# Optimization experiments

Measured on AMD Instinct MI355X. Metric: run time of the kernel, lower is better.

Reference implementation:

```python
import jax, jax.numpy as jnp
import numpy as np
import math

B, S, H = 2, 1024, 768
NH = 12
DH = H // NH  # 64


def _heads(t):
    # (B,S,H) -> (B,NH,S,DH)
    b, s, _ = t.shape
    return t.reshape(b, s, NH, DH).transpose(0, 2, 1, 3)


def _merge(t):
    # (B,NH,S,DH) -> (B,S,H)
    b, nh, s, dh = t.shape
    return t.transpose(0, 2, 1, 3).reshape(b, s, nh * dh)


def _forward(x, y, vq_w, vq_b, vk_w, vk_b, vv_w, vv_b,
             dq_w, dq_b, dk_w, dk_b, dv_w, dv_b,
             van_fc_w, van_fc_b, WD_w, d_theta_w, d_theta_b, WV_w,
             diff_fc_w, diff_fc_b, v_gamma_w, v_gamma_b,
             diff_out_w, diff_out_b, van_out_w, van_out_b,
             diff_fus_w, diff_fus_b, van_fus_w, van_fus_b,
             gate_w, nf_w, nf_b, nf_out_w, final_w, final_b):
    scale = 1.0 / math.sqrt(DH)

    # ---- Vanilla attention (dropout is eval-mode identity) ----
    q = _heads(x @ vq_w + vq_b)
    k = _heads(y @ vk_w + vk_b)
    v = _heads(y @ vv_w + vv_b)
    scores = jnp.einsum('bhid,bhjd->bhij', q, k) * scale
    probs = jax.nn.softmax(scores, axis=-1)
    van_vector = _merge(jnp.einsum('bhij,bhjd->bhid', probs, v))

    # ---- Differential attention ----
    # scores[b,h,i,j] = sum_d (q[b,h,i,d] - k[b,h,i,d]) / sqrt(DH)  (constant over j,
    # due to the module's broadcast indexing). Keep explicit softmax for exact math/vjp.
    dq = _heads(x @ dq_w + dq_b)
    dk = _heads(y @ dk_w + dk_b)
    dv = _heads(y @ dv_w + dv_b)
    s_row = (dq.sum(-1) - dk.sum(-1)) * scale  # (B,NH,S)
    d_scores = jnp.broadcast_to(s_row[..., None], s_row.shape + (s_row.shape[-1],))
    d_probs = jax.nn.softmax(d_scores, axis=-1)
    diff_vector = _merge(jnp.einsum('bhij,bhjd->bhid', d_probs, dv))

    # ---- Coupled gating (SoftMax over dim=1 == sequence axis) ----
    theta = jnp.tanh(jnp.concatenate((diff_vector @ WD_w, x_lin(van_vector, van_fc_w, van_fc_b)), axis=-1))
    d_theta = diff_vector * jax.nn.softmax(theta @ d_theta_w + d_theta_b, axis=1)
    gamma = jnp.tanh(jnp.concatenate((van_vector @ WV_w, d_theta @ diff_fc_w + diff_fc_b), axis=-1))
    a_gamma = van_vector * jax.nn.softmax(gamma @ v_gamma_w + v_gamma_b, axis=1)
    diff_out = jnp.tanh(jnp.concatenate((diff_vector, d_theta), axis=-1) @ diff_out_w + diff_out_b)
    van_out = jnp.tanh(jnp.concatenate((van_vector, a_gamma), axis=-1) @ van_out_w + van_out_b)
    diff_fusion = jnp.tanh(diff_out @ diff_fus_w + diff_fus_b)
    van_fusion = jnp.tanh(van_out @ van_fus_w + van_fus_b)
    gate = jax.nn.sigmoid(jnp.concatenate((diff_fusion, van_fusion), axis=-1) @ gate_w)  # (B,S,1)
    fusion = gate * van_fusion + (1.0 - gate) * diff_fusion
    nf = jax.nn.sigmoid(jnp.concatenate((van_vector, fusion @ nf_w + nf_b), axis=-1) @ nf_out_w)
    return nf * jnp.tanh(fusion @ final_w + final_b)


def x_lin(t, w, b):
    return t @ w + b


def setup_inputs() -> dict:
    key = jax.random.key(0)
    ks = iter(jax.random.split(key, 64))
    def w(*shape):
        return jax.random.normal(next(ks), shape, jnp.float32) * 0.02
    def b(n):
        return jnp.zeros((n,), jnp.float32)
    inp = {
        'x': jax.random.normal(next(ks), (B, S, H), jnp.float32),
        'y': jax.random.normal(next(ks), (B, S, H), jnp.float32),
        'vq_w': w(H, H), 'vq_b': b(H), 'vk_w': w(H, H), 'vk_b': b(H), 'vv_w': w(H, H), 'vv_b': b(H),
        'dq_w': w(H, H), 'dq_b': b(H), 'dk_w': w(H, H), 'dk_b': b(H), 'dv_w': w(H, H), 'dv_b': b(H),
        'van_fc_w': w(H, H), 'van_fc_b': b(H),
        'WD_w': w(H, H),
        'd_theta_w': w(2 * H, H), 'd_theta_b': b(H),
        'WV_w': w(H, H),
        'diff_fc_w': w(H, H), 'diff_fc_b': b(H),
        'v_gamma_w': w(2 * H, H), 'v_gamma_b': b(H),
        'diff_out_w': w(2 * H, H), 'diff_out_b': b(H),
        'van_out_w': w(2 * H, H), 'van_out_b': b(H),
        'diff_fus_w': w(H, H), 'diff_fus_b': b(H),
        'van_fus_w': w(H, H), 'van_fus_b': b(H),
        'gate_w': w(2 * H, 1),
        'nf_w': w(H, H), 'nf_b': b(H),
        'nf_out_w': w(2 * H, 1),
        'final_w': w(H, H), 'final_b': b(H),
    }
    return inp


def reference(x, y, vq_w, vq_b, vk_w, vk_b, vv_w, vv_b,
              dq_w, dq_b, dk_w, dk_b, dv_w, dv_b,
              van_fc_w, van_fc_b, WD_w, d_theta_w, d_theta_b, WV_w,
              diff_fc_w, diff_fc_b, v_gamma_w, v_gamma_b,
              diff_out_w, diff_out_b, van_out_w, van_out_b,
              diff_fus_w, diff_fus_b, van_fus_w, van_fus_b,
              gate_w, nf_w, nf_b, nf_out_w, final_w, final_b):
    return _forward(x, y, vq_w, vq_b, vk_w, vk_b, vv_w, vv_b,
                    dq_w, dq_b, dk_w, dk_b, dv_w, dv_b,
                    van_fc_w, van_fc_b, WD_w, d_theta_w, d_theta_b, WV_w,
                    diff_fc_w, diff_fc_b, v_gamma_w, v_gamma_b,
                    diff_out_w, diff_out_b, van_out_w, van_out_b,
                    diff_fus_w, diff_fus_b, van_fus_w, van_fus_b,
                    gate_w, nf_w, nf_b, nf_out_w, final_w, final_b)
```

## Files before the change

kernel.cpp:

```cpp
#include <hip/hip_runtime.h>
#include <hip/hip_bf16.h>
#include <math.h>

#define H 768
#define S 1024
#define BATCH 2
#define T 2048
#define TH ((size_t)T * H)

typedef unsigned short u16;
typedef __attribute__((ext_vector_type(8))) short short8;
typedef __attribute__((ext_vector_type(4))) float f32x4;

__device__ __forceinline__ u16 f2b(float f) {
  __hip_bfloat16 h = __float2bfloat16(f);
  return *reinterpret_cast<u16*>(&h);
}
__device__ __forceinline__ float b2f(u16 u) {
  __hip_bfloat16 h = *reinterpret_cast<__hip_bfloat16*>(&u);
  return __bfloat162float(h);
}
__device__ __forceinline__ void gload16(const u16* g, u16* lds) {
  __builtin_amdgcn_global_load_lds((const __attribute__((address_space(1))) void*)g,
                                   (__attribute__((address_space(3))) void*)lds, 16, 0, 0);
}

__global__ __launch_bounds__(256) void cvt2_k(const float* __restrict__ X, const float* __restrict__ Y,
                                              u16* __restrict__ OX, u16* __restrict__ OY) {
  const float* src = blockIdx.y ? Y : X;
  u16* dst = blockIdx.y ? OY : OX;
  int i = blockIdx.x * 256 + threadIdx.x;
  float4 a = ((const float4*)src)[2 * i];
  float4 b = ((const float4*)src)[2 * i + 1];
  u16 tmp[8] = {f2b(a.x), f2b(a.y), f2b(a.z), f2b(a.w), f2b(b.x), f2b(b.y), f2b(b.z), f2b(b.w)};
  ((uint4*)dst)[i] = *(uint4*)tmp;
}

struct WprepArgs {
  const float* src[14];
  unsigned dst[14];
  int ktiles[14];
  int tstart[15];
};
__global__ __launch_bounds__(256) void wprep_k(WprepArgs a, u16* __restrict__ wt) {
  __shared__ float sT[64][68];
  int blk = blockIdx.x;
  int mi = 0;
  while (blk >= a.tstart[mi + 1]) ++mi;
  int local = blk - a.tstart[mi];
  int kt = a.ktiles[mi];
  int tn = local / kt, tk = local % kt;
  int K = kt * 64;
  const float* W = a.src[mi];
  u16* D = wt + a.dst[mi];
  int t = threadIdx.x;
  int r = t >> 2, c = (t & 3) * 16;
  const float4* srcp = (const float4*)(W + ((size_t)(tk * 64 + r)) * H + tn * 64 + c);
  float4 v0 = srcp[0], v1 = srcp[1], v2 = srcp[2], v3 = srcp[3];
  *(float4*)&sT[r][c] = v0; *(float4*)&sT[r][c + 4] = v1;
  *(float4*)&sT[r][c + 8] = v2; *(float4*)&sT[r][c + 12] = v3;
  __syncthreads();
  int n = t >> 2, kk = (t & 3) * 16;
  u16 tmp[16];
  #pragma unroll
  for (int j = 0; j < 16; ++j) tmp[j] = f2b(sT[kk + j][n]);
  uint4* dst = (uint4*)(D + ((size_t)(tn * 64 + n)) * K + tk * 64 + kk);
  dst[0] = *(uint4*)&tmp[0];
  dst[1] = *(uint4*)&tmp[8];
}

__global__ __launch_bounds__(256) void meany1_k(const float* __restrict__ Y, float* __restrict__ part) {
  int blk = blockIdx.x;
  int b = blk / 24, r = blk % 24, cc = r / 8, sc = r % 8;
  int c = cc * 256 + threadIdx.x;
  const float* yp = Y + (size_t)b * S * H + (size_t)sc * 128 * H + c;
  float s = 0.f;
  for (int j = 0; j < 128; ++j) s += yp[(size_t)j * H];
  part[(sc * 2 + b) * H + c] = s;
}
__global__ __launch_bounds__(256) void meany2_k(const float* __restrict__ part, float* __restrict__ ybar) {
  int t = blockIdx.x * 256 + threadIdx.x;
  float s = 0.f;
  int b = t / H, c = t % H;
  #pragma unroll
  for (int sc = 0; sc < 8; ++sc) s += part[(sc * 2 + b) * H + c];
  ybar[t] = s * (1.0f / 1024.0f);
}

__global__ __launch_bounds__(256) void gemv_k(const float* __restrict__ A, const float* __restrict__ W,
                                              const float* __restrict__ bias, float* __restrict__ O, int act) {
  int gid = blockIdx.x * 4 + (threadIdx.x >> 6);
  int lane = threadIdx.x & 63;
  int b = gid / H, n = gid % H;
  const float* a = A + b * H;
  float s = 0.f;
  #pragma unroll
  for (int i = 0; i < 12; ++i) {
    int k = lane + 64 * i;
    s = fmaf(a[k], W[(size_t)k * H + n], s);
  }
  #pragma unroll
  for (int off = 32; off; off >>= 1) s += __shfl_xor(s, off);
  if (lane == 0) {
    if (bias) s += bias[n];
    if (act) s = tanhf(s);
    O[gid] = s;
  }
}

struct Reg {
  const u16 *A, *W, *A2, *W2;
  const float *bias, *perbatch;
  u16* Cb; u16* CbT; float* Cf;
  int ldw, ldw2;
};
struct GArgs { Reg r0, r1, r2; int act; };

__global__ __launch_bounds__(256) void bgemm_k(GArgs ga) {
  __shared__ u16 sA[3][64 * 64];
  __shared__ u16 sB[3][64 * 64];
  int t = threadIdx.x;
  int ri = blockIdx.x / 12;
  Reg R;
  if (ri == 0) R = ga.r0; else if (ri == 1) R = ga.r1; else R = ga.r2;
  int n0 = (blockIdx.x % 12) * 64;
  int m0 = blockIdx.y * 64;
  int w = t >> 6, l = t & 63, lr = l & 15, lg = l >> 4;
  int wr = (w >> 1) * 32, wc = (w & 1) * 32;

  f32x4 acc[2][2];
  #pragma unroll
  for (int i = 0; i < 2; ++i)
    #pragma unroll
    for (int j = 0; j < 2; ++j) acc[i][j] = (f32x4){0.f, 0.f, 0.f, 0.f};

  int NT = R.A2 ? 24 : 12;

  auto stage = [&](int ti) {
    int bi = ti % 3;
    const u16* Aq = (ti < 12) ? R.A : R.A2;
    const u16* Wq = (ti < 12) ? R.W : R.W2;
    int ldwq = (ti < 12) ? R.ldw : R.ldw2;
    int k0 = (ti % 12) * 64;
    #pragma unroll
    for (int ii = 0; ii < 2; ++ii) {
      int chunk = w * 128 + ii * 64 + l;
      int rr = chunk >> 3, c8 = chunk & 7;
      gload16(Aq + (size_t)(m0 + rr) * H + k0 + 8 * (c8 ^ (rr & 7)), &sA[bi][0] + (w * 128 + ii * 64) * 8);
      gload16(Wq + (size_t)(n0 + rr) * ldwq + k0 + 8 * (c8 ^ (rr & 7)), &sB[bi][0] + (w * 128 + ii * 64) * 8);
    }
  };

  stage(0);
  stage(1);
  for (int kt = 0; kt < NT; ++kt) {
    if (kt + 1 < NT) asm volatile("s_waitcnt vmcnt(4)" ::: "memory");
    else             asm volatile("s_waitcnt vmcnt(0)" ::: "memory");
    __builtin_amdgcn_s_barrier();
    if (kt + 2 < NT) stage(kt + 2);
    const u16* sAv = &sA[kt % 3][0];
    const u16* sBv = &sB[kt % 3][0];
    #pragma unroll
    for (int kh = 0; kh < 2; ++kh) {
      short8 af[2], bfr[2];
      #pragma unroll
      for (int mi = 0; mi < 2; ++mi) {
        int row = wr + 16 * mi + lr;
        af[mi] = *(const short8*)(sAv + row * 64 + 8 * ((4 * kh + lg) ^ (row & 7)));
      }
      #pragma unroll
      for (int ni = 0; ni < 2; ++ni) {
        int row = wc + 16 * ni + lr;
        bfr[ni] = *(const short8*)(sBv + row * 64 + 8 * ((4 * kh + lg) ^ (row & 7)));
      }
      #pragma unroll
      for (int mi = 0; mi < 2; ++mi)
        #pragma unroll
        for (int ni = 0; ni < 2; ++ni)
          acc[mi][ni] = __builtin_amdgcn_mfma_f32_16x16x32_bf16(af[mi], bfr[ni], acc[mi][ni], 0, 0, 0);
    }
  }

  #pragma unroll
  for (int mi = 0; mi < 2; ++mi) {
    #pragma unroll
    for (int ni = 0; ni < 2; ++ni) {
      int col = n0 + wc + 16 * ni + lr;
      u16 tmp4[4];
      #pragma unroll
      for (int reg = 0; reg < 4; ++reg) {
        int row = m0 + wr + 16 * mi + lg * 4 + reg;
        int bb = row >> 10;
        float v = acc[mi][ni][reg];
        if (R.bias) v += R.bias[col];
        if (R.perbatch) v += R.perbatch[bb * H + col];
        if (ga.act) v = tanhf(v);
        if (R.Cb) R.Cb[(size_t)row * H + col] = f2b(v);
        if (R.Cf) R.Cf[(size_t)row * H + col] = v;
        tmp4[reg] = f2b(v);
      }
      if (R.CbT) {
        int row0 = m0 + wr + 16 * mi + lg * 4;
        int bb = row0 >> 10, tok = row0 & 1023, hh = col >> 6, dd = col & 63;
        *(unsigned long long*)&R.CbT[((size_t)((bb * 12 + hh) * 64 + dd)) * 1024 + tok] =
            *(unsigned long long*)tmp4;
      }
    }
  }
}

__global__ __launch_bounds__(256) void mattn_k(
    const u16* __restrict__ Q, const u16* __restrict__ Kg,
    const u16* __restrict__ VT, u16* __restrict__ O)
{
  __shared__ u16 sK[3][64 * 64];
  __shared__ u16 sV[3][64 * 64];
  __shared__ u16 sQ[64 * 64];
  __shared__ u16 sP[4 * 16 * 64];
  int t = threadIdx.x;
  int w = t >> 6, l = t & 63, lr = l & 15, lg = l >> 4;
  int blk = blockIdx.x;
  int b = blk / 192; int rem = blk % 192; int h = rem / 16; int q0 = (rem % 16) * 64;

  #pragma unroll
  for (int i = 0; i < 2; ++i) {
    int id = t + i * 256; int r = id >> 3, c = id & 7;
    uint4 v = *(const uint4*)(Q + ((size_t)(b * 1024 + q0 + r)) * H + h * 64 + 8 * c);
    *(uint4*)(&sQ[0] + r * 64 + 8 * (c ^ (r & 7))) = v;
  }
  asm volatile("s_waitcnt lgkmcnt(0)" ::: "memory");

  auto stageKV = [&](int ti) {
    int bi = ti % 3;
    int kv0 = ti * 64;
    #pragma unroll
    for (int ii = 0; ii < 2; ++ii) {
      int chunk = w * 128 + ii * 64 + l;
      int rr = chunk >> 3, c8 = chunk & 7;
      gload16(Kg + ((size_t)(b * 1024 + kv0 + rr)) * H + h * 64 + 8 * (c8 ^ (rr & 7)),
              &sK[bi][0] + (w * 128 + ii * 64) * 8);
      gload16(VT + ((size_t)((b * 12 + h) * 64 + rr)) * 1024 + kv0 + 8 * (c8 ^ (rr & 7)),
              &sV[bi][0] + (w * 128 + ii * 64) * 8);
    }
  };

  f32x4 oacc[4];
  #pragma unroll
  for (int i = 0; i < 4; ++i) oacc[i] = (f32x4){0.f, 0.f, 0.f, 0.f};
  float lsum[4] = {0.f, 0.f, 0.f, 0.f};

  stageKV(0);
  stageKV(1);

  for (int kt = 0; kt < 16; ++kt) {
    if (kt + 1 < 16) asm volatile("s_waitcnt vmcnt(4)" ::: "memory");
    else             asm volatile("s_waitcnt vmcnt(0)" ::: "memory");
    __builtin_amdgcn_s_barrier();
    if (kt + 2 < 16) stageKV(kt + 2);
    const u16* sKv = &sK[kt % 3][0];
    const u16* sVv = &sV[kt % 3][0];

    f32x4 sacc[4];
    #pragma unroll
    for (int i = 0; i < 4; ++i) sacc[i] = (f32x4){0.f, 0.f, 0.f, 0.f};
    #pragma unroll
    for (int kh = 0; kh < 2; ++kh) {
      int qrow = 16 * w + lr;
      short8 qf = *(const short8*)(&sQ[0] + qrow * 64 + 8 * ((4 * kh + lg) ^ (qrow & 7)));
      #pragma unroll
      for (int ns = 0; ns < 4; ++ns) {
        int krow = 16 * ns + lr;
        short8 kf = *(const short8*)(sKv + krow * 64 + 8 * ((4 * kh + lg) ^ (krow & 7)));
        sacc[ns] = __builtin_amdgcn_mfma_f32_16x16x32_bf16(qf, kf, sacc[ns], 0, 0, 0);
      }
    }

    #pragma unroll
    for (int r = 0; r < 4; ++r) {
      int q = lg * 4 + r;
      #pragma unroll
      for (int ns = 0; ns < 4; ++ns) {
        float p = __expf(sacc[ns][r] * 0.125f);
        lsum[r] += p;
        int kv = 16 * ns + lr;
        unsigned byteoff = (unsigned)(w * 2048 + q * 128 + ((kv * 2) ^ ((q & 7) << 4)));
        *(u16*)((char*)sP + byteoff) = f2b(p);
      }
    }

    #pragma unroll
    for (int kh = 0; kh < 2; ++kh) {
      short8 pf = *(const short8*)((char*)sP + w * 2048 + lr * 128 + (((4 * kh + lg) << 4) ^ ((lr & 7) << 4)));
      #pragma unroll
      for (int ds = 0; ds < 4; ++ds) {
        int vrow = 16 * ds + lr;
        short8 vf = *(const short8*)(sVv + vrow * 64 + 8 * ((4 * kh + lg) ^ (vrow & 7)));
        oacc[ds] = __builtin_amdgcn_mfma_f32_16x16x32_bf16(pf, vf, oacc[ds], 0, 0, 0);
      }
    }
  }

  #pragma unroll
  for (int r = 0; r < 4; ++r) {
    #pragma unroll
    for (int off = 1; off < 16; off <<= 1) lsum[r] += __shfl_xor(lsum[r], off);
    float inv = 1.0f / lsum[r];
    int qrow = q0 + 16 * w + lg * 4 + r;
    #pragma unroll
    for (int ds = 0; ds < 4; ++ds) {
      int d = 16 * ds + lr;
      O[((size_t)(b * 1024 + qrow)) * H + h * 64 + d] = f2b(oacc[ds][r] * inv);
    }
  }
}

__global__ __launch_bounds__(256) void colsmP_k(const u16* __restrict__ Z, float* __restrict__ part) {
  int blk = blockIdx.x;
  int b = blk >> 7, sc = blk & 127;
  int t = threadIdx.x;
  const u16* zp = Z + ((size_t)(b * 1024 + sc * 8)) * H;
  float a0 = 0.f, a1 = 0.f, a2 = 0.f;
  #pragma unroll
  for (int j = 0; j < 8; ++j) {
    a0 += __expf(b2f(zp[(size_t)j * H + t]));
    a1 += __expf(b2f(zp[(size_t)j * H + t + 256]));
    a2 += __expf(b2f(zp[(size_t)j * H + t + 512]));
  }
  float* pp = part + (size_t)blk * H;
  pp[t] = a0; pp[t + 256] = a1; pp[t + 512] = a2;
}
__global__ __launch_bounds__(256) void colsmC_k(const float* __restrict__ part, float* __restrict__ inv) {
  int idx = blockIdx.x * 256 + threadIdx.x;
  int b = idx / H, c = idx % H;
  float s = 0.f;
  for (int sc = 0; sc < 128; ++sc) s += part[(size_t)(b * 128 + sc) * H + c];
  inv[idx] = 1.0f / s;
}
__global__ __launch_bounds__(256) void colsmA_k(
    const u16* __restrict__ Z, const float* __restrict__ inv,
    const float* __restrict__ mulvec, const u16* __restrict__ mulmat, u16* __restrict__ O) {
  int blk = blockIdx.x;
  int b = blk >> 7, sc = blk & 127;
  int t = threadIdx.x;
  size_t base = ((size_t)(b * 1024 + sc * 8)) * H;
  float i0 = inv[b * H + t], i1 = inv[b * H + t + 256], i2 = inv[b * H + t + 512];
  float m0 = 0.f, m1 = 0.f, m2 = 0.f;
  if (mulvec) { m0 = mulvec[b * H + t]; m1 = mulvec[b * H + t + 256]; m2 = mulvec[b * H + t + 512]; }
  #pragma unroll
  for (int j = 0; j < 8; ++j) {
    size_t row = base + (size_t)j * H;
    float e0 = __expf(b2f(Z[row + t]));
    float e1 = __expf(b2f(Z[row + t + 256]));
    float e2 = __expf(b2f(Z[row + t + 512]));
    float u0 = mulmat ? b2f(mulmat[row + t]) : m0;
    float u1 = mulmat ? b2f(mulmat[row + t + 256]) : m1;
    float u2 = mulmat ? b2f(mulmat[row + t + 512]) : m2;
    O[row + t] = f2b(u0 * e0 * i0);
    O[row + t + 256] = f2b(u1 * e1 * i1);
    O[row + t + 512] = f2b(u2 * e2 * i2);
  }
}

__global__ __launch_bounds__(256) void gatefuse_k(
    const u16* __restrict__ DF, const u16* __restrict__ VF,
    const float* __restrict__ GW, u16* __restrict__ FU)
{
  __shared__ float red[256];
  int tok = blockIdx.x;
  int t = threadIdx.x;
  const u16* df = DF + (size_t)tok * H;
  const u16* vf = VF + (size_t)tok * H;
  float dv[3], vv[3];
  float p = 0.f;
  #pragma unroll
  for (int i = 0; i < 3; ++i) {
    int c = t + i * 256;
    dv[i] = b2f(df[c]); vv[i] = b2f(vf[c]);
    p = fmaf(dv[i], GW[c], p);
    p = fmaf(vv[i], GW[H + c], p);
  }
  red[t] = p; __syncthreads();
  for (int st = 128; st; st >>= 1) { if (t < st) red[t] += red[t + st]; __syncthreads(); }
  float g = 1.0f / (1.0f + __expf(-red[0]));
  u16* fu = FU + (size_t)tok * H;
  #pragma unroll
  for (int i = 0; i < 3; ++i) {
    int c = t + i * 256;
    fu[c] = f2b(g * vv[i] + (1.0f - g) * dv[i]);
  }
}

__global__ __launch_bounds__(256) void nffinal_k(
    const u16* __restrict__ VAN, const float* __restrict__ NP,
    const float* __restrict__ NW, const float* __restrict__ FP,
    float* __restrict__ OUT)
{
  __shared__ float red[256];
  int tok = blockIdx.x;
  int t = threadIdx.x;
  const u16* va = VAN + (size_t)tok * H;
  const float* np = NP + (size_t)tok * H;
  float p = 0.f;
  #pragma unroll
  for (int i = 0; i < 3; ++i) {
    int c = t + i * 256;
    p = fmaf(b2f(va[c]), NW[c], p);
    p = fmaf(np[c], NW[H + c], p);
  }
  red[t] = p; __syncthreads();
  for (int st = 128; st; st >>= 1) { if (t < st) red[t] += red[t + st]; __syncthreads(); }
  float nf = 1.0f / (1.0f + __expf(-red[0]));
  const float* fp = FP + (size_t)tok * H;
  float* o = OUT + (size_t)tok * H;
  #pragma unroll
  for (int i = 0; i < 3; ++i) {
    int c = t + i * 256;
    o[c] = nf * tanhf(fp[c]);
  }
}

extern "C" void kernel_launch(void* const* d_in, const int* in_sizes, int n_in,
                              void* d_out, int out_size, void* d_ws, size_t ws_size,
                              hipStream_t stream) {
  const float* x        = (const float*)d_in[0];
  const float* y        = (const float*)d_in[1];
  const float* vq_w     = (const float*)d_in[2];
  const float* vq_b     = (const float*)d_in[3];
  const float* vk_w     = (const float*)d_in[4];
  const float* vk_b     = (const float*)d_in[5];
  const float* vv_w     = (const float*)d_in[6];
  const float* vv_b     = (const float*)d_in[7];
  const float* dv_w     = (const float*)d_in[12];
  const float* dv_b     = (const float*)d_in[13];
  const float* van_fc_w = (const float*)d_in[14];
  const float* van_fc_b = (const float*)d_in[15];
  const float* d_theta_w= (const float*)d_in[17];
  const float* WV_w     = (const float*)d_in[19];
  const float* diff_fc_w= (const float*)d_in[20];
  const float* diff_fc_b= (const float*)d_in[21];
  const float* v_gamma_w= (const float*)d_in[22];
  const float* diff_out_w=(const float*)d_in[24];
  const float* diff_out_b=(const float*)d_in[25];
  const float* van_out_w= (const float*)d_in[26];
  const float* van_out_b= (const float*)d_in[27];
  const float* diff_fus_w=(const float*)d_in[28];
  const float* diff_fus_b=(const float*)d_in[29];
  const float* van_fus_w= (const float*)d_in[30];
  const float* van_fus_b= (const float*)d_in[31];
  const float* gate_w   = (const float*)d_in[32];
  const float* nf_w     = (const float*)d_in[33];
  const float* nf_b     = (const float*)d_in[34];
  const float* nf_out_w = (const float*)d_in[35];
  const float* final_w  = (const float*)d_in[36];
  const float* final_b  = (const float*)d_in[37];
  float* out = (float*)d_out;

  u16* wt = (u16*)d_ws;
  const size_t HH_ = (size_t)H * H;
  const size_t HH2 = 2 * HH_;
  size_t woff[14];
  const float* wsrc[14] = {vq_w, vk_w, vv_w, van_fc_w, WV_w, diff_fc_w, diff_fus_w, van_fus_w,
                           nf_w, final_w, d_theta_w, v_gamma_w, diff_out_w, van_out_w};
  int wk[14] = {12,12,12,12,12,12,12,12,12,12, 24,24,24,24};
  size_t o = 0;
  for (int i = 0; i < 14; ++i) { woff[i] = o; o += (i < 10) ? HH_ : HH2; }
  u16* bufs = wt + o;
  u16* bX   = bufs + 0 * TH;
  u16* bY   = bufs + 1 * TH;
  u16* bQ   = bufs + 2 * TH;
  u16* bK   = bufs + 3 * TH;
  u16* bV   = bufs + 4 * TH;
  u16* bVT  = bufs + 5 * TH;
  u16* bVan = bufs + 6 * TH;
  float* F0 = (float*)(bufs + 7 * TH);
  float* F1 = F0 + TH;
  float* sm = F1 + TH;
  float* ybar  = sm;
  float* dvbar = sm + 1536;
  float* c2    = sm + 3072;
  float* part  = sm + 4608;
  float* colp  = sm + 4608 + 12288;
  float* cinv  = colp + 196608;

  WprepArgs wa;
  int ts = 0;
  for (int i = 0; i < 14; ++i) {
    wa.src[i] = wsrc[i];
    wa.dst[i] = (unsigned)woff[i];
    wa.ktiles[i] = wk[i];
    wa.tstart[i] = ts;
    ts += wk[i] * 12;
  }
  wa.tstart[14] = ts;
  wprep_k<<<ts, 256, 0, stream>>>(wa, wt);
  cvt2_k<<<dim3(TH / 8 / 256, 2), 256, 0, stream>>>(x, y, bX, bY);

  meany1_k<<<48, 256, 0, stream>>>(y, part);
  meany2_k<<<6, 256, 0, stream>>>(part, ybar);
  gemv_k<<<384, 256, 0, stream>>>(ybar, dv_w, dv_b, dvbar, 0);
  gemv_k<<<384, 256, 0, stream>>>(dvbar, diff_out_w, diff_out_b, c2, 0);

  const u16 *wt_vq = wt + woff[0], *wt_vk = wt + woff[1], *wt_vv = wt + woff[2],
            *wt_vanfc = wt + woff[3], *wt_WV = wt + woff[4], *wt_difffc = wt + woff[5],
            *wt_difffus = wt + woff[6], *wt_vanfus = wt + woff[7], *wt_nf = wt + woff[8],
            *wt_final = wt + woff[9], *wt_dtheta = wt + woff[10], *wt_vg = wt + woff[11],
            *wt_diffout = wt + woff[12], *wt_vanout = wt + woff[13];
  #define NO nullptr
  Reg RZ = {NO, NO, NO, NO, NO, NO, NO, NO, NO, 0, 0};

  {
    GArgs g;
    g.r0 = {bX, wt_vq, NO, NO, vq_b, NO, bQ, NO, NO, H, 0};
    g.r1 = {bY, wt_vk, NO, NO, vk_b, NO, bK, NO, NO, H, 0};
    g.r2 = {bY, wt_vv, NO, NO, vv_b, NO, NO, bVT, NO, H, 0};
    g.act = 0;
    bgemm_k<<<dim3(36, 32), 256, 0, stream>>>(g);
  }
  mattn_k<<<384, 256, 0, stream>>>(bQ, bK, bVT, bVan);

  {
    GArgs g;
    g.r0 = {bVan, wt_vanfc, NO, NO, van_fc_b, NO, bX, NO, NO, H, 0};
    g.r1 = {bVan, wt_WV, NO, NO, NO, NO, bK, NO, NO, H, 0};
    g.r2 = RZ;
    g.act = 1;
    bgemm_k<<<dim3(24, 32), 256, 0, stream>>>(g);
  }
  {
    GArgs g;
    g.r0 = {bX, wt_dtheta + H, NO, NO, NO, NO, bY, NO, NO, 2 * H, 0};
    g.r1 = RZ; g.r2 = RZ;
    g.act = 0;
    bgemm_k<<<dim3(12, 32), 256, 0, stream>>>(g);
  }
  colsmP_k<<<256, 256, 0, stream>>>(bY, colp);
  colsmC_k<<<6, 256, 0, stream>>>(colp, cinv);
  colsmA_k<<<256, 256, 0, stream>>>(bY, cinv, dvbar, NO, bQ);
  {
    GArgs g;
    g.r0 = {bQ, wt_difffc, NO, NO, diff_fc_b, NO, bV, NO, NO, H, 0};
    g.r1 = {bQ, wt_diffout + H, NO, NO, NO, c2, bY, NO, NO, 2 * H, 0};
    g.r2 = RZ;
    g.act = 1;
    bgemm_k<<<dim3(24, 32), 256, 0, stream>>>(g);
  }
  {
    GArgs g;
    g.r0 = {bK, wt_vg, bV, wt_vg + H, NO, NO, bX, NO, NO, 2 * H, 2 * H};
    g.r1 = RZ; g.r2 = RZ;
    g.act = 0;
    bgemm_k<<<dim3(12, 32), 256, 0, stream>>>(g);
  }
  colsmP_k<<<256, 256, 0, stream>>>(bX, colp);
  colsmC_k<<<6, 256, 0, stream>>>(colp, cinv);
  colsmA_k<<<256, 256, 0, stream>>>(bX, cinv, NO, bVan, bX);
  {
    GArgs g;
    g.r0 = {bVan, wt_vanout, bX, wt_vanout + H, van_out_b, NO, bK, NO, NO, 2 * H, 2 * H};
    g.r1 = {bY, wt_difffus, NO, NO, diff_fus_b, NO, bQ, NO, NO, H, 0};
    g.r2 = RZ;
    g.act = 1;
    bgemm_k<<<dim3(24, 32), 256, 0, stream>>>(g);
  }
  {
    GArgs g;
    g.r0 = {bK, wt_vanfus, NO, NO, van_fus_b, NO, bV, NO, NO, H, 0};
    g.r1 = RZ; g.r2 = RZ;
    g.act = 1;
    bgemm_k<<<dim3(12, 32), 256, 0, stream>>>(g);
  }
  gatefuse_k<<<T, 256, 0, stream>>>(bQ, bV, gate_w, bY);
  {
    GArgs g;
    g.r0 = {bY, wt_nf, NO, NO, nf_b, NO, NO, NO, F0, H, 0};
    g.r1 = {bY, wt_final, NO, NO, final_b, NO, NO, NO, F1, H, 0};
    g.r2 = RZ;
    g.act = 0;
    bgemm_k<<<dim3(24, 32), 256, 0, stream>>>(g);
  }
  nffinal_k<<<T, 256, 0, stream>>>(bVan, F0, nf_out_w, F1, out);
}
```

Baseline: 252.7 us.

## Fuse column-softmax partial sums into GEMM epilogue and drop two kernels

The GEMM epilogue now computes exp of each bf16-rounded output and reduces it per column across the tile, writing per-64-row partial sums. The apply kernel folds the remaining 32-way reduction and the reciprocal inline. This removes the separate partial-sum and combine kernels, along with an extra read of the logits matrix, in both softmax stages. In exchange the apply kernel repeats the 32-partial reduction in every block, and the GEMM epilogue does extra exp work.

New measurement: 232.9 us. -7.8%, faster.

```diff
diff --git a/kernel.cpp b/kernel.cpp
--- a/kernel.cpp
+++ b/kernel.cpp
@@ -111,7 +111,7 @@
 struct Reg {
   const u16 *A, *W, *A2, *W2;
   const float *bias, *perbatch;
-  u16* Cb; u16* CbT; float* Cf;
+  u16* Cb; u16* CbT; float* Cf; float* colPart;
   int ldw, ldw2;
 };
 struct GArgs { Reg r0, r1, r2; int act; };
@@ -181,6 +181,7 @@
     }
   }
 
+  float ps[2] = {0.f, 0.f};
   #pragma unroll
   for (int mi = 0; mi < 2; ++mi) {
     #pragma unroll
@@ -195,15 +196,28 @@
         if (R.bias) v += R.bias[col];
         if (R.perbatch) v += R.perbatch[bb * H + col];
         if (ga.act) v = tanhf(v);
-        if (R.Cb) R.Cb[(size_t)row * H + col] = f2b(v);
+        tmp4[reg] = f2b(v);
+        if (R.Cb) R.Cb[(size_t)row * H + col] = tmp4[reg];
         if (R.Cf) R.Cf[(size_t)row * H + col] = v;
-        tmp4[reg] = f2b(v);
+        if (R.colPart) ps[ni] += __expf(b2f(tmp4[reg]));
       }
       if (R.CbT) {
         int row0 = m0 + wr + 16 * mi + lg * 4;
         int bb = row0 >> 10, tok = row0 & 1023, hh = col >> 6, dd = col & 63;
         *(unsigned long long*)&R.CbT[((size_t)((bb * 12 + hh) * 64 + dd)) * 1024 + tok] =
             *(unsigned long long*)tmp4;
+      }
+    }
+  }
+  if (R.colPart) {
+    #pragma unroll
+    for (int ni = 0; ni < 2; ++ni) {
+      float p = ps[ni];
+      p += __shfl_xor(p, 16);
+      p += __shfl_xor(p, 32);
+      if (lg == 0) {
+        int col = n0 + wc + 16 * ni + lr;
+        R.colPart[(size_t)(blockIdx.y * 2 + (wr >> 5)) * H + col] = p;
       }
     }
   }
@@ -314,36 +328,19 @@
   }
 }
 
-__global__ __launch_bounds__(256) void colsmP_k(const u16* __restrict__ Z, float* __restrict__ part) {
-  int blk = blockIdx.x;
-  int b = blk >> 7, sc = blk & 127;
-  int t = threadIdx.x;
-  const u16* zp = Z + ((size_t)(b * 1024 + sc * 8)) * H;
-  float a0 = 0.f, a1 = 0.f, a2 = 0.f;
-  #pragma unroll
-  for (int j = 0; j < 8; ++j) {
-    a0 += __expf(b2f(zp[(size_t)j * H + t]));
-    a1 += __expf(b2f(zp[(size_t)j * H + t + 256]));
-    a2 += __expf(b2f(zp[(size_t)j * H + t + 512]));
-  }
-  float* pp = part + (size_t)blk * H;
-  pp[t] = a0; pp[t + 256] = a1; pp[t + 512] = a2;
-}
-__global__ __launch_bounds__(256) void colsmC_k(const float* __restrict__ part, float* __restrict__ inv) {
-  int idx = blockIdx.x * 256 + threadIdx.x;
-  int b = idx / H, c = idx % H;
-  float s = 0.f;
-  for (int sc = 0; sc < 128; ++sc) s += part[(size_t)(b * 128 + sc) * H + c];
-  inv[idx] = 1.0f / s;
-}
 __global__ __launch_bounds__(256) void colsmA_k(
-    const u16* __restrict__ Z, const float* __restrict__ inv,
+    const u16* __restrict__ Z, const float* __restrict__ part,
     const float* __restrict__ mulvec, const u16* __restrict__ mulmat, u16* __restrict__ O) {
   int blk = blockIdx.x;
   int b = blk >> 7, sc = blk & 127;
   int t = threadIdx.x;
+  float s0 = 0.f, s1 = 0.f, s2 = 0.f;
+  for (int i = b * 32; i < b * 32 + 32; ++i) {
+    const float* pp = part + (size_t)i * H;
+    s0 += pp[t]; s1 += pp[t + 256]; s2 += pp[t + 512];
+  }
+  float i0 = 1.0f / s0, i1 = 1.0f / s1, i2 = 1.0f / s2;
   size_t base = ((size_t)(b * 1024 + sc * 8)) * H;
-  float i0 = inv[b * H + t], i1 = inv[b * H + t + 256], i2 = inv[b * H + t + 512];
   float m0 = 0.f, m1 = 0.f, m2 = 0.f;
   if (mulvec) { m0 = mulvec[b * H + t]; m1 = mulvec[b * H + t + 256]; m2 = mulvec[b * H + t + 512]; }
   #pragma unroll
@@ -480,7 +477,6 @@
   float* c2    = sm + 3072;
   float* part  = sm + 4608;
   float* colp  = sm + 4608 + 12288;
-  float* cinv  = colp + 196608;
 
   WprepArgs wa;
   int ts = 0;
@@ -506,13 +502,13 @@
             *wt_final = wt + woff[9], *wt_dtheta = wt + woff[10], *wt_vg = wt + woff[11],
             *wt_diffout = wt + woff[12], *wt_vanout = wt + woff[13];
   #define NO nullptr
-  Reg RZ = {NO, NO, NO, NO, NO, NO, NO, NO, NO, 0, 0};
-
-  {
-    GArgs g;
-    g.r0 = {bX, wt_vq, NO, NO, vq_b, NO, bQ, NO, NO, H, 0};
-    g.r1 = {bY, wt_vk, NO, NO, vk_b, NO, bK, NO, NO, H, 0};
-    g.r2 = {bY, wt_vv, NO, NO, vv_b, NO, NO, bVT, NO, H, 0};
+  Reg RZ = {NO, NO, NO, NO, NO, NO, NO, NO, NO, NO, 0, 0};
+
+  {
+    GArgs g;
+    g.r0 = {bX, wt_vq, NO, NO, vq_b, NO, bQ, NO, NO, NO, H, 0};
+    g.r1 = {bY, wt_vk, NO, NO, vk_b, NO, bK, NO, NO, NO, H, 0};
+    g.r2 = {bY, wt_vv, NO, NO, vv_b, NO, NO, bVT, NO, NO, H, 0};
     g.act = 0;
     bgemm_k<<<dim3(36, 32), 256, 0, stream>>>(g);
   }
@@ -520,51 +516,47 @@
 
   {
     GArgs g;
-    g.r0 = {bVan, wt_vanfc, NO, NO, van_fc_b, NO, bX, NO, NO, H, 0};
-    g.r1 = {bVan, wt_WV, NO, NO, NO, NO, bK, NO, NO, H, 0};
+    g.r0 = {bVan, wt_vanfc, NO, NO, van_fc_b, NO, bX, NO, NO, NO, H, 0};
+    g.r1 = {bVan, wt_WV, NO, NO, NO, NO, bK, NO, NO, NO, H, 0};
     g.r2 = RZ;
     g.act = 1;
     bgemm_k<<<dim3(24, 32), 256, 0, stream>>>(g);
   }
   {
     GArgs g;
-    g.r0 = {bX, wt_dtheta + H, NO, NO, NO, NO, bY, NO, NO, 2 * H, 0};
+    g.r0 = {bX, wt_dtheta + H, NO, NO, NO, NO, bY, NO, NO, colp, 2 * H, 0};
     g.r1 = RZ; g.r2 = RZ;
     g.act = 0;
     bgemm_k<<<dim3(12, 32), 256, 0, stream>>>(g);
   }
-  colsmP_k<<<256, 256, 0, stream>>>(bY, colp);
-  colsmC_k<<<6, 256, 0, stream>>>(colp, cinv);
-  colsmA_k<<<256, 256, 0, stream>>>(bY, cinv, dvbar, NO, bQ);
-  {
-    GArgs g;
-    g.r0 = {bQ, wt_difffc, NO, NO, diff_fc_b, NO, bV, NO, NO, H, 0};
-    g.r1 = {bQ, wt_diffout + H, NO, NO, NO, c2, bY, NO, NO, 2 * H, 0};
+  colsmA_k<<<256, 256, 0, stream>>>(bY, colp, dvbar, NO, bQ);
+  {
+    GArgs g;
+    g.r0 = {bQ, wt_difffc, NO, NO, diff_fc_b, NO, bV, NO, NO, NO, H, 0};
+    g.r1 = {bQ, wt_diffout + H, NO, NO, NO, c2, bY, NO, NO, NO, 2 * H, 0};
     g.r2 = RZ;
     g.act = 1;
     bgemm_k<<<dim3(24, 32), 256, 0, stream>>>(g);
   }
   {
     GArgs g;
-    g.r0 = {bK, wt_vg, bV, wt_vg + H, NO, NO, bX, NO, NO, 2 * H, 2 * H};
+    g.r0 = {bK, wt_vg, bV, wt_vg + H, NO, NO, bX, NO, NO, colp, 2 * H, 2 * H};
     g.r1 = RZ; g.r2 = RZ;
     g.act = 0;
     bgemm_k<<<dim3(12, 32), 256, 0, stream>>>(g);
   }
-  colsmP_k<<<256, 256, 0, stream>>>(bX, colp);
-  colsmC_k<<<6, 256, 0, stream>>>(colp, cinv);
-  colsmA_k<<<256, 256, 0, stream>>>(bX, cinv, NO, bVan, bX);
-  {
-    GArgs g;
-    g.r0 = {bVan, wt_vanout, bX, wt_vanout + H, van_out_b, NO, bK, NO, NO, 2 * H, 2 * H};
-    g.r1 = {bY, wt_difffus, NO, NO, diff_fus_b, NO, bQ, NO, NO, H, 0};
+  colsmA_k<<<256, 256, 0, stream>>>(bX, colp, NO, bVan, bX);
+  {
+    GArgs g;
+    g.r0 = {bVan, wt_vanout, bX, wt_vanout + H, van_out_b, NO, bK, NO, NO, NO, 2 * H, 2 * H};
+    g.r1 = {bY, wt_difffus, NO, NO, diff_fus_b, NO, bQ, NO, NO, NO, H, 0};
     g.r2 = RZ;
     g.act = 1;
     bgemm_k<<<dim3(24, 32), 256, 0, stream>>>(g);
   }
   {
     GArgs g;
-    g.r0 = {bK, wt_vanfus, NO, NO, van_fus_b, NO, bV, NO, NO, H, 0};
+    g.r0 = {bK, wt_vanfus, NO, NO, van_fus_b, NO, bV, NO, NO, NO, H, 0};
     g.r1 = RZ; g.r2 = RZ;
     g.act = 1;
     bgemm_k<<<dim3(12, 32), 256, 0, stream>>>(g);
@@ -572,8 +564,8 @@
   gatefuse_k<<<T, 256, 0, stream>>>(bQ, bV, gate_w, bY);
   {
     GArgs g;
-    g.r0 = {bY, wt_nf, NO, NO, nf_b, NO, NO, NO, F0, H, 0};
-    g.r1 = {bY, wt_final, NO, NO, final_b, NO, NO, NO, F1, H, 0};
+    g.r0 = {bY, wt_nf, NO, NO, nf_b, NO, NO, NO, F0, NO, H, 0};
+    g.r1 = {bY, wt_final, NO, NO, final_b, NO, NO, NO, F1, NO, H, 0};
     g.r2 = RZ;
     g.act = 0;
     bgemm_k<<<dim3(24, 32), 256, 0, stream>>>(g);
```
